# Kernel tuning notes

Measured on AMD Instinct MI355X. Metric: run time of the kernel, lower is better.

The kernel has to match this reference:

```python
import jax, jax.numpy as jnp
import numpy as np

B, N, H, E, L = 64, 100, 128, 128, 3  # batch, nodes, node_hidden, edge_hidden, gcn layers


def setup_inputs() -> dict:
    key = jax.random.key(0)
    ks = jax.random.split(key, 12)
    s = 0.05
    return dict(
        node=jax.random.normal(ks[0], (B, N, 2), jnp.float32),
        demand=jax.random.uniform(ks[1], (B, N), jnp.float32),
        dis=jax.random.uniform(ks[2], (B, N, N), jnp.float32),
        Wn0=jax.random.normal(ks[3], (3, H), jnp.float32) * s,
        bn0=jnp.zeros((H,), jnp.float32),
        Ws=jax.random.normal(ks[4], (L, H, H), jnp.float32) * s,
        Wngh=jax.random.normal(ks[5], (L, H, H), jnp.float32) * s,
        We=jax.random.normal(ks[6], (E,), jnp.float32) * s,
        be=jnp.zeros((E,), jnp.float32),
        Wih=jax.random.normal(ks[7], (2, H, 3 * H), jnp.float32) * s,
        Whh=jax.random.normal(ks[8], (2, H, 3 * H), jnp.float32) * s,
        bih=jnp.zeros((2, 3 * H), jnp.float32),
        bhh=jnp.zeros((2, 3 * H), jnp.float32),
        Wq=jax.random.normal(ks[9], (H, H), jnp.float32) * s,
        Wc=jax.random.normal(ks[10], (E, 2), jnp.float32) * s,
        bc=jnp.zeros((2,), jnp.float32),
    )


def _gru(xin, h, Wih, Whh, bih, bhh):
    gi = xin @ Wih + bih
    gh = h @ Whh + bhh
    ir, iz, inn = jnp.split(gi, 3, -1)
    hr, hz, hn = jnp.split(gh, 3, -1)
    r = jax.nn.sigmoid(ir + hr)
    z = jax.nn.sigmoid(iz + hz)
    n = jnp.tanh(inn + r * hn)
    return (1.0 - z) * n + z * h


def _decode(x, Wih, Whh, bih, bhh, Wq, sample, key):
    b, n, h = x.shape
    scale = 1.0 / np.sqrt(h).astype(np.float32)

    def step(carry, _):
        last, hid, k = carry
        emb = x[jnp.arange(b), last]                      # [b,h]
        h0 = _gru(emb, hid[0], Wih[0], Whh[0], bih[0], bhh[0])
        h1 = _gru(h0, hid[1], Wih[1], Whh[1], bih[1], bhh[1])
        logits = jnp.einsum('bh,bnh->bn', h1 @ Wq, x) * scale
        logp = jax.nn.log_softmax(logits, -1)
        k, sk = jax.random.split(k)
        if sample:
            ind = jax.random.categorical(sk, logits)
        else:
            ind = jnp.argmax(logits, -1)
        ind = ind.astype(jnp.int32)
        chosen = jnp.take_along_axis(logp, ind[:, None], 1)[:, 0]
        return (ind, jnp.stack([h0, h1]), k), (ind, chosen)

    init = (jnp.zeros((b,), jnp.int32), jnp.zeros((2, b, h), x.dtype), key)
    _, (inds, lps) = jax.lax.scan(step, init, None, length=n - 1)
    solution = jnp.concatenate([jnp.zeros((b, 1), jnp.int32), inds.T], axis=1)  # depot 0 first
    return lps.T, solution  # logprob [b,n-1], solution [b,n]


def _count_dist(sol, dis):
    bidx = jnp.arange(sol.shape[0])[:, None]
    return dis[bidx, sol[:, :-1], sol[:, 1:]].sum(axis=1, keepdims=True)  # [b,1]


def reference(node, demand, dis, Wn0, bn0, Ws, Wngh, We, be, Wih, Whh, bih, bhh, Wq, Wc, bc):
    # --- GCN encoder ---
    h = jax.nn.relu(jnp.concatenate([node, demand[..., None]], -1) @ Wn0 + bn0)  # [B,N,H]
    A = jax.nn.softmax(-dis, -1)  # distance-based soft adjacency
    for l in range(Ws.shape[0]):
        h = jax.nn.relu(h @ Ws[l] + jnp.einsum('bij,bjh->bih', A, h @ Wngh[l]))
    e = jax.nn.relu(dis[..., None] * We + be)  # [B,N,N,E]

    key = jax.random.key(42)
    k1, _ = jax.random.split(key)
    sample_logprob, sample_solution = _decode(h, Wih, Whh, bih, bhh, Wq, True, k1)
    sample_distance = _count_dist(sample_solution, dis)
    _, greedy_solution = _decode(h, Wih, Whh, bih, bhh, Wq, False, k1)
    greedy_distance = _count_dist(greedy_solution, dis)

    predict_matrix = jax.nn.softmax(e @ Wc + bc, -1)  # [B,N,N,2]

    b, n = h.shape[0], h.shape[1]
    bidx = jnp.arange(b)[:, None]
    greedy_solution_matrix = (
        jnp.zeros((b, n, n), jnp.int32)
        .at[bidx, greedy_solution[:, :-1], greedy_solution[:, 1:]]
        .set(1)
    )
    return (sample_logprob, sample_distance, greedy_distance, predict_matrix, greedy_solution_matrix)
```

## Files before the change

kernel.cpp:

```cpp
#include <hip/hip_runtime.h>
#include <math.h>

#define BB 64
#define NN 100
#define HH 128
#define T3 384

#define O0 0
#define O1 6336
#define O2 6400
#define O3 6464
#define O4 1286464

#define TINYF 1.17549435e-38f
#define SCALEF 0.08838834764831845f

__device__ __forceinline__ unsigned rotl32(unsigned x, int d) {
    return (x << d) | (x >> (32 - d));
}

__device__ __forceinline__ void tf2x32(unsigned ks0, unsigned ks1,
                                       unsigned x0, unsigned x1,
                                       unsigned& o0, unsigned& o1) {
    unsigned ks2 = ks0 ^ ks1 ^ 0x1BD11BDAu;
    x0 += ks0; x1 += ks1;
    x0 += x1; x1 = rotl32(x1, 13); x1 ^= x0;
    x0 += x1; x1 = rotl32(x1, 15); x1 ^= x0;
    x0 += x1; x1 = rotl32(x1, 26); x1 ^= x0;
    x0 += x1; x1 = rotl32(x1, 6);  x1 ^= x0;
    x0 += ks1; x1 += ks2 + 1u;
    x0 += x1; x1 = rotl32(x1, 17); x1 ^= x0;
    x0 += x1; x1 = rotl32(x1, 29); x1 ^= x0;
    x0 += x1; x1 = rotl32(x1, 16); x1 ^= x0;
    x0 += x1; x1 = rotl32(x1, 24); x1 ^= x0;
    x0 += ks2; x1 += ks0 + 2u;
    x0 += x1; x1 = rotl32(x1, 13); x1 ^= x0;
    x0 += x1; x1 = rotl32(x1, 15); x1 ^= x0;
    x0 += x1; x1 = rotl32(x1, 26); x1 ^= x0;
    x0 += x1; x1 = rotl32(x1, 6);  x1 ^= x0;
    x0 += ks0; x1 += ks1 + 3u;
    x0 += x1; x1 = rotl32(x1, 17); x1 ^= x0;
    x0 += x1; x1 = rotl32(x1, 29); x1 ^= x0;
    x0 += x1; x1 = rotl32(x1, 16); x1 ^= x0;
    x0 += x1; x1 = rotl32(x1, 24); x1 ^= x0;
    x0 += ks1; x1 += ks2 + 4u;
    x0 += x1; x1 = rotl32(x1, 13); x1 ^= x0;
    x0 += x1; x1 = rotl32(x1, 15); x1 ^= x0;
    x0 += x1; x1 = rotl32(x1, 26); x1 ^= x0;
// ... 122 lines not shown
                          const float* __restrict__ be, const float* __restrict__ Wc,
                          const float* __restrict__ bc, float* __restrict__ out3) {
    __shared__ float sWe[128], sbe[128], sc0[128], sc1[128];
    int tid = threadIdx.x;
    if (tid < 128) {
        sWe[tid] = We[tid];
        sbe[tid] = be[tid];
        sc0[tid] = Wc[tid * 2];
        sc1[tid] = Wc[tid * 2 + 1];
    }
    __syncthreads();
    float b0 = bc[0], b1 = bc[1];
    for (int pos = blockIdx.x * 256 + tid; pos < BB * NN * NN; pos += gridDim.x * 256) {
        float d = dis[pos];
        float a0 = b0, a1 = b1;
        for (int k = 0; k < 128; k++) {
            float e = fmaxf(d * sWe[k] + sbe[k], 0.0f);
            a0 += e * sc0[k];
            a1 += e * sc1[k];
        }
        float m = fmaxf(a0, a1);
        float p0 = expf(a0 - m), p1 = expf(a1 - m);
        float inv = 1.0f / (p0 + p1);
        out3[pos * 2]     = p0 * inv;
        out3[pos * 2 + 1] = p1 * inv;
    }
}

__global__ void k_zero(float* __restrict__ p, int n) {
    int i = blockIdx.x * 256 + threadIdx.x;
    if (i < n) p[i] = 0.0f;
}

__device__ __forceinline__ void matvec_tile4(const float* __restrict__ W,
                                             const float* __restrict__ hp,
                                             int nk4,
                                             float* __restrict__ pg0,
                                             float* __restrict__ pg1) {
    float a00 = 0.f, a01 = 0.f, a02 = 0.f, a03 = 0.f;
    float a10 = 0.f, a11 = 0.f, a12 = 0.f, a13 = 0.f;
#pragma unroll 4
    for (int k4 = 0; k4 < nk4; ++k4) {
        float4 hA = *(const float4*)(hp + 4 * k4);
        float4 hB = *(const float4*)(hp + 132 + 4 * k4);
        const float* Wk = W + (size_t)(4 * k4) * T3;
        float4 w0 = *(const float4*)(Wk);
        float4 w1 = *(const float4*)(Wk + T3);
        float4 w2 = *(const float4*)(Wk + 2 * T3);
        float4 w3 = *(const float4*)(Wk + 3 * T3);
        a00 += hA.x * w0.x; a01 += hA.x * w0.y; a02 += hA.x * w0.z; a03 += hA.x * w0.w;
        a10 += hB.x * w0.x; a11 += hB.x * w0.y; a12 += hB.x * w0.z; a13 += hB.x * w0.w;
        a00 += hA.y * w1.x; a01 += hA.y * w1.y; a02 += hA.y * w1.z; a03 += hA.y * w1.w;
        a10 += hB.y * w1.x; a11 += hB.y * w1.y; a12 += hB.y * w1.z; a13 += hB.y * w1.w;
        a00 += hA.z * w2.x; a01 += hA.z * w2.y; a02 += hA.z * w2.z; a03 += hA.z * w2.w;
        a10 += hB.z * w2.x; a11 += hB.z * w2.y; a12 += hB.z * w2.z; a13 += hB.z * w2.w;
        a00 += hA.w * w3.x; a01 += hA.w * w3.y; a02 += hA.w * w3.z; a03 += hA.w * w3.w;
        a10 += hB.w * w3.x; a11 += hB.w * w3.y; a12 += hB.w * w3.z; a13 += hB.w * w3.w;
    }
    float4 o;
    o.x = a00; o.y = a01; o.z = a02; o.w = a03;
    *(float4*)pg0 = o;
    o.x = a10; o.y = a11; o.z = a12; o.w = a13;
    *(float4*)pg1 = o;
}

__global__ __launch_bounds__(512, 2) void k_decode4(
    const float* __restrict__ P0,
    const float* __restrict__ Z,
    const float* __restrict__ dis,
    const float* __restrict__ Wih,
    const float* __restrict__ Whh,
    const float* __restrict__ bih,
    const float* __restrict__ bhh,
    float* __restrict__ out) {
    __shared__ float Zs[NN * 132];
    __shared__ float h0s[2 * 132], h1s[2 * 132];
    __shared__ float gi0s[2 * 384];
    __shared__ float pgA[2 * 2 * 392];
    __shared__ float pgB[2 * 2 * 392];
    __shared__ float pgC[4 * 2 * 392];
    __shared__ float sbhh0[T3], sbih1[T3], sbhh1[T3];
    __shared__ float pl[2 * 2 * 100];
    __shared__ float gum[128];
    __shared__ int s_ind2[2];

    const int tid = threadIdx.x;
    const int b = blockIdx.x;

    const float* __restrict__ Wih1 = Wih + 128 * T3;

    for (int i4 = tid; i4 < NN * 32; i4 += 512) {
        int r = i4 >> 5, c4 = (i4 & 31) * 4;
        *(float4*)&Zs[r * 132 + c4] = *(const float4*)&Z[(b * NN + r) * 128 + c4];
    }
    if (tid < T3) {
        sbhh0[tid] = bhh[tid];
        sbih1[tid] = bih[T3 + tid];
        sbhh1[tid] = bhh[T3 + tid];
    }
    if (tid < 256) {
        int m = tid >> 7, i = tid & 127;
        h0s[m * 132 + i] = 0.0f;
        h1s[m * 132 + i] = 0.0f;
    }
    if (tid == 0) { s_ind2[0] = 0; s_ind2[1] = 0; }

    unsigned kk0, kk1;
    tf2x32(0u, 42u, 0u, 0u, kk0, kk1);

    int lastm = 0;
    float dist = 0.0f;
    __syncthreads();

    for (int t = 0; t < NN - 1; t++) {
        if (tid < 384) {
            const int unit = tid / 192;
            const int r = tid - unit * 192;
            const int ks = r / 96, j4 = r - ks * 96;
            const int j0 = j4 * 4, k0 = ks * 64;
            const float* W = Whh + unit * (128 * T3) + (size_t)k0 * T3 + j0;
            const float* hp = ((unit == 0) ? h0s : h1s) + k0;
            float* pg = (unit == 0) ? pgA : pgB;
            matvec_tile4(W, hp, 16,
                         &pg[(ks * 2 + 0) * 392 + j0],
                         &pg[(ks * 2 + 1) * 392 + j0]);
        } else {
            int u = tid - 384;
            int l0 = s_ind2[0], l1 = s_ind2[1];
#pragma unroll
            for (int q = 0; q < 6; q++) {
                int f = u + 128 * q;
                int m = (f >= 384) ? 1 : 0;
                int j = f - m * 384;
                gi0s[f] = P0[(size_t)(b * NN + (m ? l1 : l0)) * T3 + j];
            }
            unsigned sk0, sk1, nk0, nk1;
            tf2x32(kk0, kk1, 0u, 1u, sk0, sk1);
            tf2x32(kk0, kk1, 0u, 0u, nk0, nk1);
            kk0 = nk0; kk1 = nk1;
            if (u < NN) gum[u] = gumbel_f(sk0, sk1, (unsigned)(b * NN + u));
        }
        __syncthreads();

        if (tid < 256) {
            int m = tid >> 7, i = tid & 127;
            float ghr = pgA[(0 * 2 + m) * 392 + i]       + pgA[(1 * 2 + m) * 392 + i]       + sbhh0[i];
            float ghz = pgA[(0 * 2 + m) * 392 + i + 128] + pgA[(1 * 2 + m) * 392 + i + 128] + sbhh0[i + 128];
            float ghn = pgA[(0 * 2 + m) * 392 + i + 256] + pgA[(1 * 2 + m) * 392 + i + 256] + sbhh0[i + 256];
            float rr = 1.0f / (1.0f + expf(-(gi0s[m * 384 + i] + ghr)));
            float zz = 1.0f / (1.0f + expf(-(gi0s[m * 384 + i + 128] + ghz)));
            float nn = tanhf(gi0s[m * 384 + i + 256] + rr * ghn);
            h0s[m * 132 + i] = (1.0f - zz) * nn + zz * h0s[m * 132 + i];
        }
        __syncthreads();

        if (tid < 384) {
            const int ks = tid / 96, j4 = tid - ks * 96;
            const int j0 = j4 * 4, k0 = ks * 32;
            const float* W = Wih1 + (size_t)k0 * T3 + j0;
            matvec_tile4(W, h0s + k0, 8,
                         &pgC[(ks * 2 + 0) * 392 + j0],
                         &pgC[(ks * 2 + 1) * 392 + j0]);
        }
        __syncthreads();

        if (tid < 256) {
            int m = tid >> 7, i = tid & 127;
            float gir = sbih1[i], giz = sbih1[i + 128], gin = sbih1[i + 256];
#pragma unroll
            for (int ks = 0; ks < 4; ks++) {
                int pb = (ks * 2 + m) * 392;
                gir += pgC[pb + i];
                giz += pgC[pb + i + 128];
                gin += pgC[pb + i + 256];
            }
            float ghr = pgB[(0 * 2 + m) * 392 + i]       + pgB[(1 * 2 + m) * 392 + i]       + sbhh1[i];
            float ghz = pgB[(0 * 2 + m) * 392 + i + 128] + pgB[(1 * 2 + m) * 392 + i + 128] + sbhh1[i + 128];
            float ghn = pgB[(0 * 2 + m) * 392 + i + 256] + pgB[(1 * 2 + m) * 392 + i + 256] + sbhh1[i + 256];
            float rr = 1.0f / (1.0f + expf(-(gir + ghr)));
            float zz = 1.0f / (1.0f + expf(-(giz + ghz)));
            float nn = tanhf(gin + rr * ghn);
            h1s[m * 132 + i] = (1.0f - zz) * nn + zz * h1s[m * 132 + i];
        }
        __syncthreads();

        if (tid < 200) {
            int ks = tid / 100, n = tid - ks * 100;
            int k0 = ks * 64;
            const float* Zp = &Zs[n * 132 + k0];
            const float* hp = &h1s[k0];
            float a0 = 0.f, a1 = 0.f;
#pragma unroll 4
            for (int q = 0; q < 16; q++) {
                float4 z4 = *(const float4*)(Zp + 4 * q);
                float4 hA = *(const float4*)(hp + 4 * q);
                float4 hB = *(const float4*)(hp + 132 + 4 * q);
                a0 += hA.x * z4.x; a0 += hA.y * z4.y; a0 += hA.z * z4.z; a0 += hA.w * z4.w;
                a1 += hB.x * z4.x; a1 += hB.y * z4.y; a1 += hB.z * z4.z; a1 += hB.w * z4.w;
            }
            pl[(0 * 2 + ks) * 100 + n] = a0;
            pl[(1 * 2 + ks) * 100 + n] = a1;
        }
        __syncthreads();

        if (tid < 128) {
            const int m = tid >> 6, lane = tid & 63;
            float v0, v1 = -__builtin_inff();
            v0 = (pl[(m * 2 + 0) * 100 + lane] + pl[(m * 2 + 1) * 100 + lane]) * SCALEF;
            if (lane + 64 < NN)
                v1 = (pl[(m * 2 + 0) * 100 + lane + 64] + pl[(m * 2 + 1) * 100 + lane + 64]) * SCALEF;
            float mx = fmaxf(v0, v1);
            for (int off = 32; off > 0; off >>= 1) mx = fmaxf(mx, __shfl_xor(mx, off));
            float e = expf(v0 - mx) + ((lane + 64 < NN) ? expf(v1 - mx) : 0.0f);
            for (int off = 32; off > 0; off >>= 1) e += __shfl_xor(e, off);
            float a0 = v0, a1 = v1;
            if (m == 0) {
                a0 += gum[lane];
                if (lane + 64 < NN) a1 += gum[lane + 64];
            }
            float bv; int bi;
            if (a1 > a0) { bv = a1; bi = lane + 64; } else { bv = a0; bi = lane; }
            for (int off = 32; off > 0; off >>= 1) {
                float ov = __shfl_xor(bv, off);
                int   oi = __shfl_xor(bi, off);
                if (ov > bv || (ov == bv && oi < bi)) { bv = ov; bi = oi; }
            }
            int ind = bi;
            float la = __shfl(v0, ind & 63);
            float lb = __shfl(v1, ind & 63);
            float lv = (ind < 64) ? la : lb;
            if (lane == 0) {
                if (m == 0) out[O0 + b * (NN - 1) + t] = lv - mx - logf(e);
                else        out[O4 + (size_t)b * NN * NN + lastm * NN + ind] = 1.0f;
                s_ind2[m] = ind;
            }
            dist += dis[b * NN * NN + lastm * NN + ind];
            lastm = ind;
        }
        __syncthreads();
    }

    if (tid == 0)  out[O1 + b] = dist;
    if (tid == 64) out[O2 + b] = dist;
}

__global__ __launch_bounds__(768) void k_decode2(
    const float* __restrict__ P0, const float* __restrict__ Z,
    const float* __restrict__ dis,
    const float* __restrict__ Wih, const float* __restrict__ Whh,
    const float* __restrict__ bih, const float* __restrict__ bhh,
    float* __restrict__ out) {
    __shared__ float Zs[NN * 129];
    __shared__ float h0s[128], h1s[128];
    __shared__ float gi0s[T3];
    __shared__ float pg0[2 * T3];
    __shared__ float gi1s[T3], gh1s[T3];
    __shared__ float sbhh0[T3], sbih1[T3], sbhh1[T3];
    __shared__ float plx[4 * NN];
    __shared__ float logits[NN];
    __shared__ float s_m, s_s;
    __shared__ int s_ind;

    const int tid = threadIdx.x;
    const int b = blockIdx.x >> 1;
    const int greedy = blockIdx.x & 1;

    const float* Whh0 = Whh;
    const float* Wih1 = Wih + 128 * T3;
    const float* Whh1 = Whh + 128 * T3;

    for (int idx = tid; idx < NN * 128; idx += 768) {
        int r = idx >> 7, c = idx & 127;
        Zs[r * 129 + c] = Z[(b * NN + r) * 128 + c];
    }
    if (tid < T3) {
        sbhh0[tid] = bhh[tid];
        sbih1[tid] = bih[T3 + tid];
        sbhh1[tid] = bhh[T3 + tid];
    }
    if (tid < 128) { h0s[tid] = 0.0f; h1s[tid] = 0.0f; }

    unsigned kk0, kk1;
    tf2x32(0u, 42u, 0u, 0u, kk0, kk1);

    int last = 0;
    float dist = 0.0f;
    __syncthreads();

    for (int t = 0; t < NN - 1; t++) {
        unsigned sk0, sk1, nk0, nk1;
        tf2x32(kk0, kk1, 0u, 1u, sk0, sk1);
        tf2x32(kk0, kk1, 0u, 0u, nk0, nk1);
        kk0 = nk0; kk1 = nk1;

        {
            const float* P0row = P0 + (size_t)(b * NN + last) * T3;
            if (tid < T3) {
                int j = tid;
                float acc = 0.0f;
                for (int k = 0; k < 64; k++) acc += h0s[k] * Whh0[k * T3 + j];
                pg0[j] = acc;
                gi0s[j] = P0row[j];
            } else {
                int j = tid - T3;
                float acc = 0.0f;
                for (int k = 64; k < 128; k++) acc += h0s[k] * Whh0[k * T3 + j];
                pg0[T3 + j] = acc;
            }
        }
        __syncthreads();
        if (tid < 128) {
            float ghr = pg0[tid] + pg0[T3 + tid] + sbhh0[tid];
            float ghz = pg0[tid + 128] + pg0[T3 + tid + 128] + sbhh0[tid + 128];
            float ghn = pg0[tid + 256] + pg0[T3 + tid + 256] + sbhh0[tid + 256];
            float r = 1.0f / (1.0f + expf(-(gi0s[tid] + ghr)));
            float z = 1.0f / (1.0f + expf(-(gi0s[tid + 128] + ghz)));
            float n = tanhf(gi0s[tid + 256] + r * ghn);
            h0s[tid] = (1.0f - z) * n + z * h0s[tid];
        }
        __syncthreads();
        if (tid < T3) {
            int j = tid;
            float acc = sbih1[j];
            for (int k = 0; k < 128; k++) acc += h0s[k] * Wih1[k * T3 + j];
            gi1s[j] = acc;
        } else {
            int j = tid - T3;
            float acc = sbhh1[j];
            for (int k = 0; k < 128; k++) acc += h1s[k] * Whh1[k * T3 + j];
            gh1s[j] = acc;
        }
        __syncthreads();
        if (tid < 128) {
            float r = 1.0f / (1.0f + expf(-(gi1s[tid] + gh1s[tid])));
            float z = 1.0f / (1.0f + expf(-(gi1s[tid + 128] + gh1s[tid + 128])));
            float n = tanhf(gi1s[tid + 256] + r * gh1s[tid + 256]);
            h1s[tid] = (1.0f - z) * n + z * h1s[tid];
        }
        __syncthreads();
        if (tid < 400) {
            int n = tid % 100, p = tid / 100;
            int k0 = p * 32;
            float acc = 0.0f;
            for (int kk = 0; kk < 32; kk++) acc += h1s[k0 + kk] * Zs[n * 129 + k0 + kk];
            plx[p * 100 + n] = acc;
        }
        __syncthreads();
        if (tid < 64) {
            float v0 = -__builtin_inff(), v1 = -__builtin_inff();
            {
                int n = tid;
                v0 = (plx[n] + plx[100 + n] + plx[200 + n] + plx[300 + n]) * SCALEF;
                logits[n] = v0;
            }
            if (tid + 64 < NN) {
                int n = tid + 64;
                v1 = (plx[n] + plx[100 + n] + plx[200 + n] + plx[300 + n]) * SCALEF;
                logits[n] = v1;
            }
            float m = fmaxf(v0, v1);
            for (int off = 32; off > 0; off >>= 1) m = fmaxf(m, __shfl_xor(m, off));
            float e = expf(v0 - m) + ((tid + 64 < NN) ? expf(v1 - m) : 0.0f);
            for (int off = 32; off > 0; off >>= 1) e += __shfl_xor(e, off);
            float a0 = v0, a1 = v1;
            if (!greedy) {
                a0 = v0 + gumbel_f(sk0, sk1, (unsigned)(b * NN + tid));
                if (tid + 64 < NN) a1 = v1 + gumbel_f(sk0, sk1, (unsigned)(b * NN + tid + 64));
            }
            float bv; int bi;
            if (a1 > a0) { bv = a1; bi = tid + 64; } else { bv = a0; bi = tid; }
            for (int off = 32; off > 0; off >>= 1) {
                float ov = __shfl_xor(bv, off);
                int   oi = __shfl_xor(bi, off);
                if (ov > bv || (ov == bv && oi < bi)) { bv = ov; bi = oi; }
            }
            if (tid == 0) { s_m = m; s_s = e; s_ind = bi; }
        }
        __syncthreads();
        int ind = s_ind;
        if (tid == 0) {
            if (!greedy) out[O0 + b * (NN - 1) + t] = logits[ind] - s_m - logf(s_s);
            dist += dis[b * NN * NN + last * NN + ind];
            if (greedy) out[O4 + b * NN * NN + last * NN + ind] = 1.0f;
        }
        last = ind;
        __syncthreads();
    }
    if (tid == 0) {
        if (!greedy) out[O1 + b] = dist;
        else         out[O2 + b] = dist;
    }
}

extern "C" void kernel_launch(void* const* d_in, const int* in_sizes, int n_in,
                              void* d_out, int out_size, void* d_ws, size_t ws_size,
                              hipStream_t stream) {
    (void)in_sizes; (void)n_in; (void)out_size;
    const float* node   = (const float*)d_in[0];
    const float* demand = (const float*)d_in[1];
    const float* dis    = (const float*)d_in[2];
    const float* Wn0    = (const float*)d_in[3];
    const float* bn0    = (const float*)d_in[4];
    const float* Ws     = (const float*)d_in[5];
    const float* Wngh   = (const float*)d_in[6];
    const float* We     = (const float*)d_in[7];
    const float* be     = (const float*)d_in[8];
    const float* Wih    = (const float*)d_in[9];
    const float* Whh    = (const float*)d_in[10];
    const float* bih    = (const float*)d_in[11];
    const float* bhh    = (const float*)d_in[12];
    const float* Wq     = (const float*)d_in[13];
    const float* Wc     = (const float*)d_in[14];
    const float* bc     = (const float*)d_in[15];
    float* out = (float*)d_out;
    float* ws  = (float*)d_ws;

    float* hA  = ws;
    float* hB  = ws + 819200;
    float* hw  = ws + 1638400;
    float* A   = ws + 2457600;
    float* P0  = ws + 2457600;
    float* WqT = ws + 4915200;
    const size_t need_bytes = (size_t)4931584 * 4;
    const bool big_ws = ws_size >= need_bytes;

    hipLaunchKernelGGL(k_embed, dim3(3200), dim3(256), 0, stream, node, demand, Wn0, bn0, hA);
    hipLaunchKernelGGL(k_adj, dim3(6400), dim3(64), 0, stream, dis, A);

    float* cur = hA;
    float* nxt = hB;
    for (int l = 0; l < 3; l++) {
        hipLaunchKernelGGL(k_hw, dim3(800), dim3(256), 0, stream, cur, Wngh + l * 16384, hw);
        hipLaunchKernelGGL(k_agg, dim3(1600), dim3(256), 0, stream, cur, Ws + l * 16384, A, hw, nxt);
        float* tswap = cur; cur = nxt; nxt = tswap;
    }

    hipLaunchKernelGGL(k_predict, dim3(2500), dim3(256), 0, stream, dis, We, be, Wc, bc, out + O3);
    hipLaunchKernelGGL(k_zero, dim3(2500), dim3(256), 0, stream, out + O4, BB * NN * NN);

    hipLaunchKernelGGL(k_transpose128, dim3(64), dim3(256), 0, stream, Wq, WqT);
    hipLaunchKernelGGL(k_hw, dim3(800), dim3(256), 0, stream, cur, WqT, hw);
    hipLaunchKernelGGL(k_mm384, dim3(800, 3), dim3(256), 0, stream, cur, Wih, bih, P0);
    if (big_ws) {
        hipLaunchKernelGGL(k_decode4, dim3(64), dim3(512), 0, stream,
                           P0, hw, dis, Wih, Whh, bih, bhh, out);
    } else {
        hipLaunchKernelGGL(k_decode2, dim3(128), dim3(768), 0, stream,
                           P0, hw, dis, Wih, Whh, bih, bhh, out);
    }
}
```

Baseline: 979.8 us.

## Keep recurrent GRU weights resident in registers across decode steps

The decode kernel now has each of 512 threads load a 16x6 slice of both Whh matrices into registers once, instead of re-reading them from global memory every step. The matvec work is repartitioned into 8 k-groups by 64 j-groups, with the partial sums reduced in shared memory. The Gumbel noise and the P0 prefetch move into other phases so all threads share the matvec work. Holding 192 floats per thread raises register pressure under launch_bounds(512,2), which risks spilling, and the larger partial-sum buffers use more shared memory.

```diff
diff --git a/kernel.cpp b/kernel.cpp
--- a/kernel.cpp
+++ b/kernel.cpp
@@ -202,39 +202,7 @@
     if (i < n) p[i] = 0.0f;
 }
 
-__device__ __forceinline__ void matvec_tile4(const float* __restrict__ W,
-                                             const float* __restrict__ hp,
-                                             int nk4,
-                                             float* __restrict__ pg0,
-                                             float* __restrict__ pg1) {
-    float a00 = 0.f, a01 = 0.f, a02 = 0.f, a03 = 0.f;
-    float a10 = 0.f, a11 = 0.f, a12 = 0.f, a13 = 0.f;
-#pragma unroll 4
-    for (int k4 = 0; k4 < nk4; ++k4) {
-        float4 hA = *(const float4*)(hp + 4 * k4);
-        float4 hB = *(const float4*)(hp + 132 + 4 * k4);
-        const float* Wk = W + (size_t)(4 * k4) * T3;
-        float4 w0 = *(const float4*)(Wk);
-        float4 w1 = *(const float4*)(Wk + T3);
-        float4 w2 = *(const float4*)(Wk + 2 * T3);
-        float4 w3 = *(const float4*)(Wk + 3 * T3);
-        a00 += hA.x * w0.x; a01 += hA.x * w0.y; a02 += hA.x * w0.z; a03 += hA.x * w0.w;
-        a10 += hB.x * w0.x; a11 += hB.x * w0.y; a12 += hB.x * w0.z; a13 += hB.x * w0.w;
-        a00 += hA.y * w1.x; a01 += hA.y * w1.y; a02 += hA.y * w1.z; a03 += hA.y * w1.w;
-        a10 += hB.y * w1.x; a11 += hB.y * w1.y; a12 += hB.y * w1.z; a13 += hB.y * w1.w;
-        a00 += hA.z * w2.x; a01 += hA.z * w2.y; a02 += hA.z * w2.z; a03 += hA.z * w2.w;
-        a10 += hB.z * w2.x; a11 += hB.z * w2.y; a12 += hB.z * w2.z; a13 += hB.z * w2.w;
-        a00 += hA.w * w3.x; a01 += hA.w * w3.y; a02 += hA.w * w3.z; a03 += hA.w * w3.w;
-        a10 += hB.w * w3.x; a11 += hB.w * w3.y; a12 += hB.w * w3.z; a13 += hB.w * w3.w;
-    }
-    float4 o;
-    o.x = a00; o.y = a01; o.z = a02; o.w = a03;
-    *(float4*)pg0 = o;
-    o.x = a10; o.y = a11; o.z = a12; o.w = a13;
-    *(float4*)pg1 = o;
-}
-
-__global__ __launch_bounds__(512, 2) void k_decode4(
+__global__ __launch_bounds__(512, 2) void k_decode5(
     const float* __restrict__ P0,
     const float* __restrict__ Z,
     const float* __restrict__ dis,
@@ -246,9 +214,8 @@
     __shared__ float Zs[NN * 132];
     __shared__ float h0s[2 * 132], h1s[2 * 132];
     __shared__ float gi0s[2 * 384];
-    __shared__ float pgA[2 * 2 * 392];
-    __shared__ float pgB[2 * 2 * 392];
-    __shared__ float pgC[4 * 2 * 392];
+    __shared__ float pgA[8 * 2 * 392];
+    __shared__ float pgB[8 * 2 * 392];
     __shared__ float sbhh0[T3], sbih1[T3], sbhh1[T3];
     __shared__ float pl[2 * 2 * 100];
     __shared__ float gum[128];
@@ -256,8 +223,27 @@
 
     const int tid = threadIdx.x;
     const int b = blockIdx.x;
+    const int kg = tid >> 6;
+    const int jg = tid & 63;
+    const int k0 = kg * 16, j0 = jg * 6;
 
     const float* __restrict__ Wih1 = Wih + 128 * T3;
+
+    float wA[16][6], wB[16][6];
+    {
+        const float* WAp = Whh + (size_t)k0 * T3 + j0;
+        const float* WBp = Whh + 128 * T3 + (size_t)k0 * T3 + j0;
+#pragma unroll
+        for (int k = 0; k < 16; k++) {
+#pragma unroll
+            for (int q = 0; q < 3; q++) {
+                float2 a = *(const float2*)(WAp + (size_t)k * T3 + 2 * q);
+                wA[k][2 * q] = a.x; wA[k][2 * q + 1] = a.y;
+                float2 c = *(const float2*)(WBp + (size_t)k * T3 + 2 * q);
+                wB[k][2 * q] = c.x; wB[k][2 * q + 1] = c.y;
+            }
+        }
+    }
 
     for (int i4 = tid; i4 < NN * 32; i4 += 512) {
         int r = i4 >> 5, c4 = (i4 & 31) * 4;
@@ -283,40 +269,84 @@
     __syncthreads();
 
     for (int t = 0; t < NN - 1; t++) {
+        unsigned sk0, sk1, nkA, nkB;
+        tf2x32(kk0, kk1, 0u, 1u, sk0, sk1);
+        tf2x32(kk0, kk1, 0u, 0u, nkA, nkB);
+        kk0 = nkA; kk1 = nkB;
+
+        float pf0 = 0.f, pf1 = 0.f;
+        int pf_m = 0, pf_j = 0;
         if (tid < 384) {
-            const int unit = tid / 192;
-            const int r = tid - unit * 192;
-            const int ks = r / 96, j4 = r - ks * 96;
-            const int j0 = j4 * 4, k0 = ks * 64;
-            const float* W = Whh + unit * (128 * T3) + (size_t)k0 * T3 + j0;
-            const float* hp = ((unit == 0) ? h0s : h1s) + k0;
-            float* pg = (unit == 0) ? pgA : pgB;
-            matvec_tile4(W, hp, 16,
-                         &pg[(ks * 2 + 0) * 392 + j0],
-                         &pg[(ks * 2 + 1) * 392 + j0]);
-        } else {
-            int u = tid - 384;
-            int l0 = s_ind2[0], l1 = s_ind2[1];
-#pragma unroll
-            for (int q = 0; q < 6; q++) {
-                int f = u + 128 * q;
-                int m = (f >= 384) ? 1 : 0;
-                int j = f - m * 384;
-                gi0s[f] = P0[(size_t)(b * NN + (m ? l1 : l0)) * T3 + j];
-            }
-            unsigned sk0, sk1, nk0, nk1;
-            tf2x32(kk0, kk1, 0u, 1u, sk0, sk1);
-            tf2x32(kk0, kk1, 0u, 0u, nk0, nk1);
-            kk0 = nk0; kk1 = nk1;
-            if (u < NN) gum[u] = gumbel_f(sk0, sk1, (unsigned)(b * NN + u));
+            pf_m = (tid >= 192);
+            pf_j = (tid - pf_m * 192) * 2;
+            float2 g2 = *(const float2*)&P0[(size_t)(b * NN + s_ind2[pf_m]) * T3 + pf_j];
+            pf0 = g2.x; pf1 = g2.y;
+        }
+
+        {
+            float acc0[6], acc1[6];
+#pragma unroll
+            for (int j = 0; j < 6; j++) { acc0[j] = 0.f; acc1[j] = 0.f; }
+#pragma unroll
+            for (int q = 0; q < 4; q++) {
+                float4 ha = *(const float4*)&h0s[k0 + 4 * q];
+                float4 hb = *(const float4*)&h0s[132 + k0 + 4 * q];
+#pragma unroll
+                for (int j = 0; j < 6; j++) {
+                    acc0[j] += wA[4 * q + 0][j] * ha.x + wA[4 * q + 1][j] * ha.y
+                             + wA[4 * q + 2][j] * ha.z + wA[4 * q + 3][j] * ha.w;
+                    acc1[j] += wA[4 * q + 0][j] * hb.x + wA[4 * q + 1][j] * hb.y
+                             + wA[4 * q + 2][j] * hb.z + wA[4 * q + 3][j] * hb.w;
+                }
+            }
+#pragma unroll
+            for (int q = 0; q < 3; q++) {
+                float2 o0; o0.x = acc0[2 * q]; o0.y = acc0[2 * q + 1];
+                *(float2*)&pgA[(kg * 2 + 0) * 392 + j0 + 2 * q] = o0;
+                float2 o1; o1.x = acc1[2 * q]; o1.y = acc1[2 * q + 1];
+                *(float2*)&pgA[(kg * 2 + 1) * 392 + j0 + 2 * q] = o1;
+            }
+        }
+        {
+            float acc0[6], acc1[6];
+#pragma unroll
+            for (int j = 0; j < 6; j++) { acc0[j] = 0.f; acc1[j] = 0.f; }
+#pragma unroll
+            for (int q = 0; q < 4; q++) {
+                float4 ha = *(const float4*)&h1s[k0 + 4 * q];
+                float4 hb = *(const float4*)&h1s[132 + k0 + 4 * q];
+#pragma unroll
+                for (int j = 0; j < 6; j++) {
+                    acc0[j] += wB[4 * q + 0][j] * ha.x + wB[4 * q + 1][j] * ha.y
+                             + wB[4 * q + 2][j] * ha.z + wB[4 * q + 3][j] * ha.w;
+                    acc1[j] += wB[4 * q + 0][j] * hb.x + wB[4 * q + 1][j] * hb.y
+                             + wB[4 * q + 2][j] * hb.z + wB[4 * q + 3][j] * hb.w;
+                }
+            }
+#pragma unroll
+            for (int q = 0; q < 3; q++) {
+                float2 o0; o0.x = acc0[2 * q]; o0.y = acc0[2 * q + 1];
+                *(float2*)&pgB[(kg * 2 + 0) * 392 + j0 + 2 * q] = o0;
+                float2 o1; o1.x = acc1[2 * q]; o1.y = acc1[2 * q + 1];
+                *(float2*)&pgB[(kg * 2 + 1) * 392 + j0 + 2 * q] = o1;
+            }
+        }
+        if (tid < 384) {
+            gi0s[pf_m * 384 + pf_j] = pf0;
+            gi0s[pf_m * 384 + pf_j + 1] = pf1;
         }
         __syncthreads();
 
         if (tid < 256) {
             int m = tid >> 7, i = tid & 127;
-            float ghr = pgA[(0 * 2 + m) * 392 + i]       + pgA[(1 * 2 + m) * 392 + i]       + sbhh0[i];
-            float ghz = pgA[(0 * 2 + m) * 392 + i + 128] + pgA[(1 * 2 + m) * 392 + i + 128] + sbhh0[i + 128];
-            float ghn = pgA[(0 * 2 + m) * 392 + i + 256] + pgA[(1 * 2 + m) * 392 + i + 256] + sbhh0[i + 256];
+            float ghr = sbhh0[i], ghz = sbhh0[i + 128], ghn = sbhh0[i + 256];
+#pragma unroll
+            for (int g = 0; g < 8; g++) {
+                int pb = (g * 2 + m) * 392;
+                ghr += pgA[pb + i];
+                ghz += pgA[pb + i + 128];
+                ghn += pgA[pb + i + 256];
+            }
             float rr = 1.0f / (1.0f + expf(-(gi0s[m * 384 + i] + ghr)));
             float zz = 1.0f / (1.0f + expf(-(gi0s[m * 384 + i + 128] + ghz)));
             float nn = tanhf(gi0s[m * 384 + i + 256] + rr * ghn);
@@ -324,29 +354,54 @@
         }
         __syncthreads();
 
-        if (tid < 384) {
-            const int ks = tid / 96, j4 = tid - ks * 96;
-            const int j0 = j4 * 4, k0 = ks * 32;
-            const float* W = Wih1 + (size_t)k0 * T3 + j0;
-            matvec_tile4(W, h0s + k0, 8,
-                         &pgC[(ks * 2 + 0) * 392 + j0],
-                         &pgC[(ks * 2 + 1) * 392 + j0]);
+        {
+            float acc0[6], acc1[6];
+#pragma unroll
+            for (int j = 0; j < 6; j++) { acc0[j] = 0.f; acc1[j] = 0.f; }
+#pragma unroll
+            for (int q = 0; q < 4; q++) {
+                float4 ha = *(const float4*)&h0s[k0 + 4 * q];
+                float4 hb = *(const float4*)&h0s[132 + k0 + 4 * q];
+#pragma unroll
+                for (int kk2 = 0; kk2 < 4; kk2++) {
+                    const float* wp = Wih1 + (size_t)(k0 + 4 * q + kk2) * T3 + j0;
+                    float2 w01 = *(const float2*)(wp);
+                    float2 w23 = *(const float2*)(wp + 2);
+                    float2 w45 = *(const float2*)(wp + 4);
+                    float hx = (kk2 == 0) ? ha.x : (kk2 == 1) ? ha.y : (kk2 == 2) ? ha.z : ha.w;
+                    float hy = (kk2 == 0) ? hb.x : (kk2 == 1) ? hb.y : (kk2 == 2) ? hb.z : hb.w;
+                    acc0[0] += w01.x * hx; acc0[1] += w01.y * hx;
+                    acc0[2] += w23.x * hx; acc0[3] += w23.y * hx;
+                    acc0[4] += w45.x * hx; acc0[5] += w45.y * hx;
+                    acc1[0] += w01.x * hy; acc1[1] += w01.y * hy;
+                    acc1[2] += w23.x * hy; acc1[3] += w23.y * hy;
+                    acc1[4] += w45.x * hy; acc1[5] += w45.y * hy;
+                }
+            }
+#pragma unroll
+            for (int q = 0; q < 3; q++) {
+                float2 o0; o0.x = acc0[2 * q]; o0.y = acc0[2 * q + 1];
+                *(float2*)&pgA[(kg * 2 + 0) * 392 + j0 + 2 * q] = o0;
+                float2 o1; o1.x = acc1[2 * q]; o1.y = acc1[2 * q + 1];
+                *(float2*)&pgA[(kg * 2 + 1) * 392 + j0 + 2 * q] = o1;
+            }
         }
         __syncthreads();
 
         if (tid < 256) {
             int m = tid >> 7, i = tid & 127;
             float gir = sbih1[i], giz = sbih1[i + 128], gin = sbih1[i + 256];
-#pragma unroll
-            for (int ks = 0; ks < 4; ks++) {
-                int pb = (ks * 2 + m) * 392;
-                gir += pgC[pb + i];
-                giz += pgC[pb + i + 128];
-                gin += pgC[pb + i + 256];
-            }
-            float ghr = pgB[(0 * 2 + m) * 392 + i]       + pgB[(1 * 2 + m) * 392 + i]       + sbhh1[i];
-            float ghz = pgB[(0 * 2 + m) * 392 + i + 128] + pgB[(1 * 2 + m) * 392 + i + 128] + sbhh1[i + 128];
-            float ghn = pgB[(0 * 2 + m) * 392 + i + 256] + pgB[(1 * 2 + m) * 392 + i + 256] + sbhh1[i + 256];
+            float ghr = sbhh1[i], ghz = sbhh1[i + 128], ghn = sbhh1[i + 256];
+#pragma unroll
+            for (int g = 0; g < 8; g++) {
+                int pa = (g * 2 + m) * 392;
+                gir += pgA[pa + i];
+                giz += pgA[pa + i + 128];
+                gin += pgA[pa + i + 256];
+                ghr += pgB[pa + i];
+                ghz += pgB[pa + i + 128];
+                ghn += pgB[pa + i + 256];
+            }
             float rr = 1.0f / (1.0f + expf(-(gir + ghr)));
             float zz = 1.0f / (1.0f + expf(-(giz + ghz)));
             float nn = tanhf(gin + rr * ghn);
@@ -356,9 +411,9 @@
 
         if (tid < 200) {
             int ks = tid / 100, n = tid - ks * 100;
-            int k0 = ks * 64;
-            const float* Zp = &Zs[n * 132 + k0];
-            const float* hp = &h1s[k0];
+            int kk0p = ks * 64;
+            const float* Zp = &Zs[n * 132 + kk0p];
+            const float* hp = &h1s[kk0p];
             float a0 = 0.f, a1 = 0.f;
 #pragma unroll 4
             for (int q = 0; q < 16; q++) {
@@ -370,6 +425,9 @@
             }
             pl[(0 * 2 + ks) * 100 + n] = a0;
             pl[(1 * 2 + ks) * 100 + n] = a1;
+        } else if (tid >= 256 && tid < 356) {
+            int u = tid - 256;
+            gum[u] = gumbel_f(sk0, sk1, (unsigned)(b * NN + u));
         }
         __syncthreads();
 
@@ -612,7 +670,7 @@
     hipLaunchKernelGGL(k_hw, dim3(800), dim3(256), 0, stream, cur, WqT, hw);
     hipLaunchKernelGGL(k_mm384, dim3(800, 3), dim3(256), 0, stream, cur, Wih, bih, P0);
     if (big_ws) {
-        hipLaunchKernelGGL(k_decode4, dim3(64), dim3(512), 0, stream,
+        hipLaunchKernelGGL(k_decode5, dim3(64), dim3(512), 0, stream,
                            P0, hw, dis, Wih, Whh, bih, bhh, out);
     } else {
         hipLaunchKernelGGL(k_decode2, dim3(128), dim3(768), 0, stream,
```

After: 1.710 ms. 1.74x slower.

## Split each batch's decode across four cooperating blocks with global flag sync

Applied to the files above, without the earlier changes.

Adds a decode kernel in which each batch element's sequential GRU decode is spread over four blocks. Each block owns a quarter of the hidden units and exchanges partial hidden states and logits through global memory, using atomic counters as inter-block barriers twice per step. Blocks are mapped to XCDs so the four partners share one. The aim is more parallelism and shorter per-step latency than one block per batch element, at the cost of spin-wait synchronisation and a deadlock risk if all 256 blocks are not co-resident.

```diff
diff --git a/kernel.cpp b/kernel.cpp
--- a/kernel.cpp
+++ b/kernel.cpp
@@ -14,6 +14,9 @@
 
 #define TINYF 1.17549435e-38f
 #define SCALEF 0.08838834764831845f
+
+#define HIDX(k) ((((k) >> 4) * 20) + ((k) & 15))
+#define HSTR 160
 
 __device__ __forceinline__ unsigned rotl32(unsigned x, int d) {
     return (x << d) | (x >> (32 - d));
@@ -202,6 +205,306 @@
     if (i < n) p[i] = 0.0f;
 }
 
+__global__ __launch_bounds__(256, 2) void k_decode7(
+    const float* __restrict__ P0,
+    const float* __restrict__ Z,
+    const float* __restrict__ dis,
+    const float* __restrict__ Wih,
+    const float* __restrict__ Whh,
+    const float* __restrict__ bih,
+    const float* __restrict__ bhh,
+    float* __restrict__ xch,
+    unsigned* __restrict__ flags,
+    float* __restrict__ out) {
+    __shared__ float ZqT[32 * 100];
+    __shared__ float h0s[2 * HSTR], h1s[2 * HSTR];
+    __shared__ float h0q[2 * 32], h1q[2 * 32];
+    __shared__ float gi0[2 * 96];
+    __shared__ float pgA[8 * 2 * 100];
+    __shared__ float pgB[8 * 2 * 100];
+    __shared__ float pgC[8 * 2 * 100];
+    __shared__ float sb_hh0[96], sb_ih1[96], sb_hh1[96];
+    __shared__ float logits[2 * 100];
+    __shared__ float gum[100];
+    __shared__ int s_ind2[2];
+
+    const int tid = threadIdx.x;
+    const int nblk = blockIdx.x;
+    const int xcd = nblk & 7, slot = nblk >> 3;
+    const int g = xcd * 8 + (slot & 7);
+    const int s = slot >> 3;
+    const int b = g;
+
+    const float* __restrict__ Whh0 = Whh;
+    const float* __restrict__ Whh1 = Whh + 128 * T3;
+    const float* __restrict__ Wih1 = Wih + 128 * T3;
+    unsigned* flag = flags + g * 32;
+
+    const int jq = tid >> 3, ks = tid & 7;
+    const int run = jq >> 3, j4 = jq & 7;
+    const int jabs = run * 128 + 32 * s + j4 * 4;
+    const int jloc = run * 32 + j4 * 4;
+    const int kb = ks * 16;
+
+    for (int i = tid; i < 3200; i += 256) {
+        int c = i / 100, n = i - c * 100;
+        ZqT[i] = Z[(b * NN + n) * 128 + 32 * s + c];
+    }
+    if (tid < 96) {
+        int r = tid >> 5, il = tid & 31;
+        int ja = r * 128 + 32 * s + il;
+        sb_hh0[tid] = bhh[ja];
+        sb_ih1[tid] = bih[T3 + ja];
+        sb_hh1[tid] = bhh[T3 + ja];
+    }
+    if (tid < 256) {
+        int m = tid >> 7, k = tid & 127;
+        h0s[m * HSTR + HIDX(k)] = 0.0f;
+        h1s[m * HSTR + HIDX(k)] = 0.0f;
+    }
+    if (tid == 0) { s_ind2[0] = 0; s_ind2[1] = 0; }
+
+    unsigned kk0 = 0, kk1 = 0;
+    tf2x32(0u, 42u, 0u, 0u, kk0, kk1);
+
+    int lastm = 0;
+    float dist = 0.0f;
+    __syncthreads();
+
+    for (int t = 0; t < NN - 1; t++) {
+        const int par = t & 1;
+        float* xg  = xch + ((size_t)(par * 64 + g)) * 1536;
+        float* xh0 = xg;
+        float* xh1 = xg + 256;
+        float* xlp = xg + 512;
+
+        if (tid < 192) {
+            float4 hA[2][4], hB[2][4];
+#pragma unroll
+            for (int m = 0; m < 2; m++)
+#pragma unroll
+                for (int q = 0; q < 4; q++) {
+                    hA[m][q] = *(const float4*)&h0s[m * HSTR + ks * 20 + 4 * q];
+                    hB[m][q] = *(const float4*)&h1s[m * HSTR + ks * 20 + 4 * q];
+                }
+            float a0[2][4], a1[2][4];
+#pragma unroll
+            for (int m = 0; m < 2; m++)
+#pragma unroll
+                for (int j = 0; j < 4; j++) { a0[m][j] = 0.f; a1[m][j] = 0.f; }
+#pragma unroll
+            for (int q = 0; q < 4; q++) {
+#pragma unroll
+                for (int kk = 0; kk < 4; kk++) {
+                    int k = kb + 4 * q + kk;
+                    float4 w0 = *(const float4*)&Whh0[(size_t)k * T3 + jabs];
+                    float4 w1 = *(const float4*)&Whh1[(size_t)k * T3 + jabs];
+                    float hA0 = (kk == 0) ? hA[0][q].x : (kk == 1) ? hA[0][q].y : (kk == 2) ? hA[0][q].z : hA[0][q].w;
+                    float hA1 = (kk == 0) ? hA[1][q].x : (kk == 1) ? hA[1][q].y : (kk == 2) ? hA[1][q].z : hA[1][q].w;
+                    float hB0 = (kk == 0) ? hB[0][q].x : (kk == 1) ? hB[0][q].y : (kk == 2) ? hB[0][q].z : hB[0][q].w;
+                    float hB1 = (kk == 0) ? hB[1][q].x : (kk == 1) ? hB[1][q].y : (kk == 2) ? hB[1][q].z : hB[1][q].w;
+                    a0[0][0] += w0.x * hA0; a0[0][1] += w0.y * hA0; a0[0][2] += w0.z * hA0; a0[0][3] += w0.w * hA0;
+                    a0[1][0] += w0.x * hA1; a0[1][1] += w0.y * hA1; a0[1][2] += w0.z * hA1; a0[1][3] += w0.w * hA1;
+                    a1[0][0] += w1.x * hB0; a1[0][1] += w1.y * hB0; a1[0][2] += w1.z * hB0; a1[0][3] += w1.w * hB0;
+                    a1[1][0] += w1.x * hB1; a1[1][1] += w1.y * hB1; a1[1][2] += w1.z * hB1; a1[1][3] += w1.w * hB1;
+                }
+            }
+#pragma unroll
+            for (int m = 0; m < 2; m++) {
+                float4 o;
+                o.x = a0[m][0]; o.y = a0[m][1]; o.z = a0[m][2]; o.w = a0[m][3];
+                *(float4*)&pgA[(ks * 2 + m) * 100 + jloc] = o;
+                o.x = a1[m][0]; o.y = a1[m][1]; o.z = a1[m][2]; o.w = a1[m][3];
+                *(float4*)&pgB[(ks * 2 + m) * 100 + jloc] = o;
+            }
+        } else {
+            int u = tid - 192;
+            unsigned sk0, sk1, nkA, nkB;
+            tf2x32(kk0, kk1, 0u, 1u, sk0, sk1);
+            tf2x32(kk0, kk1, 0u, 0u, nkA, nkB);
+            kk0 = nkA; kk1 = nkB;
+            if (u < 48) {
+                int m = u / 24, q = u - m * 24;
+                int r = q >> 3, jj4 = q & 7;
+                int ja = r * 128 + 32 * s + jj4 * 4;
+                float4 g4 = *(const float4*)&P0[(size_t)(b * NN + s_ind2[m]) * T3 + ja];
+                *(float4*)&gi0[m * 96 + r * 32 + jj4 * 4] = g4;
+            }
+            for (int u2 = u; u2 < NN; u2 += 64)
+                gum[u2] = gumbel_f(sk0, sk1, (unsigned)(b * NN + u2));
+        }
+        __syncthreads();
+
+        if (tid < 64) {
+            int m = tid >> 5, il = tid & 31;
+            int i = 32 * s + il;
+            float ghr = sb_hh0[il], ghz = sb_hh0[32 + il], ghn = sb_hh0[64 + il];
+#pragma unroll
+            for (int k8 = 0; k8 < 8; k8++) {
+                int pb = (k8 * 2 + m) * 100;
+                ghr += pgA[pb + il];
+                ghz += pgA[pb + 32 + il];
+                ghn += pgA[pb + 64 + il];
+            }
+            float rr = 1.0f / (1.0f + expf(-(gi0[m * 96 + il] + ghr)));
+            float zz = 1.0f / (1.0f + expf(-(gi0[m * 96 + 32 + il] + ghz)));
+            float nn = tanhf(gi0[m * 96 + 64 + il] + rr * ghn);
+            float hnew = (1.0f - zz) * nn + zz * h0s[m * HSTR + HIDX(i)];
+            h0q[m * 32 + il] = hnew;
+            __hip_atomic_store(&xh0[(s * 2 + m) * 32 + il], hnew,
+                               __ATOMIC_RELAXED, __HIP_MEMORY_SCOPE_AGENT);
+        }
+        __syncthreads();
+        if (tid == 0) {
+            __hip_atomic_fetch_add(flag, 1u, __ATOMIC_ACQ_REL, __HIP_MEMORY_SCOPE_AGENT);
+            unsigned tgt = 8u * t + 4u;
+            while (__hip_atomic_load(flag, __ATOMIC_ACQUIRE, __HIP_MEMORY_SCOPE_AGENT) < tgt)
+                __builtin_amdgcn_s_sleep(2);
+        }
+        __syncthreads();
+        {
+            int ss = tid >> 6, rem = tid & 63, m = rem >> 5, il = rem & 31;
+            float v = __hip_atomic_load(&xh0[(ss * 2 + m) * 32 + il],
+                                        __ATOMIC_RELAXED, __HIP_MEMORY_SCOPE_AGENT);
+            int k = ss * 32 + il;
+            h0s[m * HSTR + HIDX(k)] = v;
+        }
+        __syncthreads();
+
+        if (tid < 192) {
+            float4 hA[2][4];
+#pragma unroll
+            for (int m = 0; m < 2; m++)
+#pragma unroll
+                for (int q = 0; q < 4; q++)
+                    hA[m][q] = *(const float4*)&h0s[m * HSTR + ks * 20 + 4 * q];
+            float a0[2][4];
+#pragma unroll
+            for (int m = 0; m < 2; m++)
+#pragma unroll
+                for (int j = 0; j < 4; j++) a0[m][j] = 0.f;
+#pragma unroll
+            for (int q = 0; q < 4; q++) {
+#pragma unroll
+                for (int kk = 0; kk < 4; kk++) {
+                    int k = kb + 4 * q + kk;
+                    float4 w = *(const float4*)&Wih1[(size_t)k * T3 + jabs];
+                    float h0v = (kk == 0) ? hA[0][q].x : (kk == 1) ? hA[0][q].y : (kk == 2) ? hA[0][q].z : hA[0][q].w;
+                    float h1v = (kk == 0) ? hA[1][q].x : (kk == 1) ? hA[1][q].y : (kk == 2) ? hA[1][q].z : hA[1][q].w;
+                    a0[0][0] += w.x * h0v; a0[0][1] += w.y * h0v; a0[0][2] += w.z * h0v; a0[0][3] += w.w * h0v;
+                    a0[1][0] += w.x * h1v; a0[1][1] += w.y * h1v; a0[1][2] += w.z * h1v; a0[1][3] += w.w * h1v;
+                }
+            }
+#pragma unroll
+            for (int m = 0; m < 2; m++) {
+                float4 o;
+                o.x = a0[m][0]; o.y = a0[m][1]; o.z = a0[m][2]; o.w = a0[m][3];
+                *(float4*)&pgC[(ks * 2 + m) * 100 + jloc] = o;
+            }
+        }
+        __syncthreads();
+
+        if (tid < 64) {
+            int m = tid >> 5, il = tid & 31;
+            int i = 32 * s + il;
+            float gir = sb_ih1[il], giz = sb_ih1[32 + il], gin = sb_ih1[64 + il];
+            float ghr = sb_hh1[il], ghz = sb_hh1[32 + il], ghn = sb_hh1[64 + il];
+#pragma unroll
+            for (int k8 = 0; k8 < 8; k8++) {
+                int pb = (k8 * 2 + m) * 100;
+                gir += pgC[pb + il];
+                giz += pgC[pb + 32 + il];
+                gin += pgC[pb + 64 + il];
+                ghr += pgB[pb + il];
+                ghz += pgB[pb + 32 + il];
+                ghn += pgB[pb + 64 + il];
+            }
+            float rr = 1.0f / (1.0f + expf(-(gir + ghr)));
+            float zz = 1.0f / (1.0f + expf(-(giz + ghz)));
+            float nn = tanhf(gin + rr * ghn);
+            float hnew = (1.0f - zz) * nn + zz * h1s[m * HSTR + HIDX(i)];
+            h1q[m * 32 + il] = hnew;
+            __hip_atomic_store(&xh1[(s * 2 + m) * 32 + il], hnew,
+                               __ATOMIC_RELAXED, __HIP_MEMORY_SCOPE_AGENT);
+        }
+        __syncthreads();
+
+        if (tid < 200) {
+            int mm = tid / 100, n = tid - mm * 100;
+            float acc = 0.0f;
+#pragma unroll 8
+            for (int c = 0; c < 32; c++)
+                acc += h1q[mm * 32 + c] * ZqT[c * 100 + n];
+            __hip_atomic_store(&xlp[(s * 2 + mm) * 100 + n], acc,
+                               __ATOMIC_RELAXED, __HIP_MEMORY_SCOPE_AGENT);
+        }
+        __syncthreads();
+        if (tid == 0) {
+            __hip_atomic_fetch_add(flag, 1u, __ATOMIC_ACQ_REL, __HIP_MEMORY_SCOPE_AGENT);
+            unsigned tgt = 8u * t + 8u;
+            while (__hip_atomic_load(flag, __ATOMIC_ACQUIRE, __HIP_MEMORY_SCOPE_AGENT) < tgt)
+                __builtin_amdgcn_s_sleep(2);
+        }
+        __syncthreads();
+        {
+            int ss = tid >> 6, rem = tid & 63, m = rem >> 5, il = rem & 31;
+            float v = __hip_atomic_load(&xh1[(ss * 2 + m) * 32 + il],
+                                        __ATOMIC_RELAXED, __HIP_MEMORY_SCOPE_AGENT);
+            int k = ss * 32 + il;
+            h1s[m * HSTR + HIDX(k)] = v;
+        }
+        if (tid < 200) {
+            int mm = tid / 100, n = tid - mm * 100;
+            float sum = 0.0f;
+#pragma unroll
+            for (int ss = 0; ss < 4; ss++)
+                sum += __hip_atomic_load(&xlp[(ss * 2 + mm) * 100 + n],
+                                         __ATOMIC_RELAXED, __HIP_MEMORY_SCOPE_AGENT);
+            logits[mm * 100 + n] = sum * SCALEF;
+        }
+        __syncthreads();
+
+        if (tid < 128) {
+            const int m = tid >> 6, lane = tid & 63;
+            float v0 = logits[m * 100 + lane];
+            float v1 = (lane + 64 < NN) ? logits[m * 100 + lane + 64] : -__builtin_inff();
+            float mx = fmaxf(v0, v1);
+            for (int off = 32; off > 0; off >>= 1) mx = fmaxf(mx, __shfl_xor(mx, off));
+            float e = expf(v0 - mx) + ((lane + 64 < NN) ? expf(v1 - mx) : 0.0f);
+            for (int off = 32; off > 0; off >>= 1) e += __shfl_xor(e, off);
+            float a0 = v0, a1 = v1;
+            if (m == 0) {
+                a0 += gum[lane];
+                if (lane + 64 < NN) a1 += gum[lane + 64];
+            }
+            float bv; int bi;
+            if (a1 > a0) { bv = a1; bi = lane + 64; } else { bv = a0; bi = lane; }
+            for (int off = 32; off > 0; off >>= 1) {
+                float ov = __shfl_xor(bv, off);
+                int   oi = __shfl_xor(bi, off);
+                if (ov > bv || (ov == bv && oi < bi)) { bv = ov; bi = oi; }
+            }
+            int ind = bi;
+            float la = __shfl(v0, ind & 63);
+            float lb = __shfl(v1, ind & 63);
+            float lv = (ind < 64) ? la : lb;
+            if (lane == 0) {
+                if (s == 0) {
+                    if (m == 0) out[O0 + b * (NN - 1) + t] = lv - mx - logf(e);
+                    else        out[O4 + (size_t)b * NN * NN + lastm * NN + ind] = 1.0f;
+                }
+                s_ind2[m] = ind;
+            }
+            dist += dis[b * NN * NN + lastm * NN + ind];
+            lastm = ind;
+        }
+        __syncthreads();
+    }
+
+    if (s == 0 && tid == 0)  out[O1 + b] = dist;
+    if (s == 0 && tid == 64) out[O2 + b] = dist;
+}
+
 __device__ __forceinline__ void matvec_tile4(const float* __restrict__ W,
                                              const float* __restrict__ hp,
                                              int nk4,
@@ -235,13 +538,10 @@
 }
 
 __global__ __launch_bounds__(512, 2) void k_decode4(
-    const float* __restrict__ P0,
-    const float* __restrict__ Z,
+    const float* __restrict__ P0, const float* __restrict__ Z,
     const float* __restrict__ dis,
-    const float* __restrict__ Wih,
-    const float* __restrict__ Whh,
-    const float* __restrict__ bih,
-    const float* __restrict__ bhh,
+    const float* __restrict__ Wih, const float* __restrict__ Whh,
+    const float* __restrict__ bih, const float* __restrict__ bhh,
     float* __restrict__ out) {
     __shared__ float Zs[NN * 132];
     __shared__ float h0s[2 * 132], h1s[2 * 132];
@@ -256,7 +556,6 @@
 
     const int tid = threadIdx.x;
     const int b = blockIdx.x;
-
     const float* __restrict__ Wih1 = Wih + 128 * T3;
 
     for (int i4 = tid; i4 < NN * 32; i4 += 512) {
@@ -356,9 +655,9 @@
 
         if (tid < 200) {
             int ks = tid / 100, n = tid - ks * 100;
-            int k0 = ks * 64;
-            const float* Zp = &Zs[n * 132 + k0];
-            const float* hp = &h1s[k0];
+            int kk0p = ks * 64;
+            const float* Zp = &Zs[n * 132 + kk0p];
+            const float* hp = &h1s[kk0p];
             float a0 = 0.f, a1 = 0.f;
 #pragma unroll 4
             for (int q = 0; q < 16; q++) {
@@ -412,154 +711,6 @@
 
     if (tid == 0)  out[O1 + b] = dist;
     if (tid == 64) out[O2 + b] = dist;
-}
-
-__global__ __launch_bounds__(768) void k_decode2(
-    const float* __restrict__ P0, const float* __restrict__ Z,
-    const float* __restrict__ dis,
-    const float* __restrict__ Wih, const float* __restrict__ Whh,
-    const float* __restrict__ bih, const float* __restrict__ bhh,
-    float* __restrict__ out) {
-    __shared__ float Zs[NN * 129];
-    __shared__ float h0s[128], h1s[128];
-    __shared__ float gi0s[T3];
-    __shared__ float pg0[2 * T3];
-    __shared__ float gi1s[T3], gh1s[T3];
-    __shared__ float sbhh0[T3], sbih1[T3], sbhh1[T3];
-    __shared__ float plx[4 * NN];
-    __shared__ float logits[NN];
-    __shared__ float s_m, s_s;
-    __shared__ int s_ind;
-
-    const int tid = threadIdx.x;
-    const int b = blockIdx.x >> 1;
-    const int greedy = blockIdx.x & 1;
-
-    const float* Whh0 = Whh;
-    const float* Wih1 = Wih + 128 * T3;
-    const float* Whh1 = Whh + 128 * T3;
-
-    for (int idx = tid; idx < NN * 128; idx += 768) {
-        int r = idx >> 7, c = idx & 127;
-        Zs[r * 129 + c] = Z[(b * NN + r) * 128 + c];
-    }
-    if (tid < T3) {
-        sbhh0[tid] = bhh[tid];
-        sbih1[tid] = bih[T3 + tid];
-        sbhh1[tid] = bhh[T3 + tid];
-    }
-    if (tid < 128) { h0s[tid] = 0.0f; h1s[tid] = 0.0f; }
-
-    unsigned kk0, kk1;
-    tf2x32(0u, 42u, 0u, 0u, kk0, kk1);
-
-    int last = 0;
-    float dist = 0.0f;
-    __syncthreads();
-
-    for (int t = 0; t < NN - 1; t++) {
-        unsigned sk0, sk1, nk0, nk1;
-        tf2x32(kk0, kk1, 0u, 1u, sk0, sk1);
-        tf2x32(kk0, kk1, 0u, 0u, nk0, nk1);
-        kk0 = nk0; kk1 = nk1;
-
-        {
-            const float* P0row = P0 + (size_t)(b * NN + last) * T3;
-            if (tid < T3) {
-                int j = tid;
-                float acc = 0.0f;
-                for (int k = 0; k < 64; k++) acc += h0s[k] * Whh0[k * T3 + j];
-                pg0[j] = acc;
-                gi0s[j] = P0row[j];
-            } else {
-                int j = tid - T3;
-                float acc = 0.0f;
-                for (int k = 64; k < 128; k++) acc += h0s[k] * Whh0[k * T3 + j];
-                pg0[T3 + j] = acc;
-            }
-        }
-        __syncthreads();
-        if (tid < 128) {
-            float ghr = pg0[tid] + pg0[T3 + tid] + sbhh0[tid];
-            float ghz = pg0[tid + 128] + pg0[T3 + tid + 128] + sbhh0[tid + 128];
-            float ghn = pg0[tid + 256] + pg0[T3 + tid + 256] + sbhh0[tid + 256];
-            float r = 1.0f / (1.0f + expf(-(gi0s[tid] + ghr)));
-            float z = 1.0f / (1.0f + expf(-(gi0s[tid + 128] + ghz)));
-            float n = tanhf(gi0s[tid + 256] + r * ghn);
-            h0s[tid] = (1.0f - z) * n + z * h0s[tid];
-        }
-        __syncthreads();
-        if (tid < T3) {
-            int j = tid;
-            float acc = sbih1[j];
-            for (int k = 0; k < 128; k++) acc += h0s[k] * Wih1[k * T3 + j];
-            gi1s[j] = acc;
-        } else {
-            int j = tid - T3;
-            float acc = sbhh1[j];
-            for (int k = 0; k < 128; k++) acc += h1s[k] * Whh1[k * T3 + j];
-            gh1s[j] = acc;
-        }
-        __syncthreads();
-        if (tid < 128) {
-            float r = 1.0f / (1.0f + expf(-(gi1s[tid] + gh1s[tid])));
-            float z = 1.0f / (1.0f + expf(-(gi1s[tid + 128] + gh1s[tid + 128])));
-            float n = tanhf(gi1s[tid + 256] + r * gh1s[tid + 256]);
-            h1s[tid] = (1.0f - z) * n + z * h1s[tid];
-        }
-        __syncthreads();
-        if (tid < 400) {
-            int n = tid % 100, p = tid / 100;
-            int k0 = p * 32;
-            float acc = 0.0f;
-            for (int kk = 0; kk < 32; kk++) acc += h1s[k0 + kk] * Zs[n * 129 + k0 + kk];
-            plx[p * 100 + n] = acc;
-        }
-        __syncthreads();
-        if (tid < 64) {
-            float v0 = -__builtin_inff(), v1 = -__builtin_inff();
-            {
-                int n = tid;
-                v0 = (plx[n] + plx[100 + n] + plx[200 + n] + plx[300 + n]) * SCALEF;
-                logits[n] = v0;
-            }
-            if (tid + 64 < NN) {
-                int n = tid + 64;
-                v1 = (plx[n] + plx[100 + n] + plx[200 + n] + plx[300 + n]) * SCALEF;
-                logits[n] = v1;
-            }
-            float m = fmaxf(v0, v1);
-            for (int off = 32; off > 0; off >>= 1) m = fmaxf(m, __shfl_xor(m, off));
-            float e = expf(v0 - m) + ((tid + 64 < NN) ? expf(v1 - m) : 0.0f);
-            for (int off = 32; off > 0; off >>= 1) e += __shfl_xor(e, off);
-            float a0 = v0, a1 = v1;
-            if (!greedy) {
-                a0 = v0 + gumbel_f(sk0, sk1, (unsigned)(b * NN + tid));
-                if (tid + 64 < NN) a1 = v1 + gumbel_f(sk0, sk1, (unsigned)(b * NN + tid + 64));
-            }
-            float bv; int bi;
-            if (a1 > a0) { bv = a1; bi = tid + 64; } else { bv = a0; bi = tid; }
-            for (int off = 32; off > 0; off >>= 1) {
-                float ov = __shfl_xor(bv, off);
-                int   oi = __shfl_xor(bi, off);
-                if (ov > bv || (ov == bv && oi < bi)) { bv = ov; bi = oi; }
-            }
-            if (tid == 0) { s_m = m; s_s = e; s_ind = bi; }
-        }
-        __syncthreads();
-        int ind = s_ind;
-        if (tid == 0) {
-            if (!greedy) out[O0 + b * (NN - 1) + t] = logits[ind] - s_m - logf(s_s);
-            dist += dis[b * NN * NN + last * NN + ind];
-            if (greedy) out[O4 + b * NN * NN + last * NN + ind] = 1.0f;
-        }
-        last = ind;
-        __syncthreads();
-    }
-    if (tid == 0) {
-        if (!greedy) out[O1 + b] = dist;
-        else         out[O2 + b] = dist;
-    }
 }
 
 extern "C" void kernel_launch(void* const* d_in, const int* in_sizes, int n_in,
@@ -585,14 +736,16 @@
     float* out = (float*)d_out;
     float* ws  = (float*)d_ws;
 
-    float* hA  = ws;
-    float* hB  = ws + 819200;
-    float* hw  = ws + 1638400;
-    float* A   = ws + 2457600;
-    float* P0  = ws + 2457600;
-    float* WqT = ws + 4915200;
-    const size_t need_bytes = (size_t)4931584 * 4;
-    const bool big_ws = ws_size >= need_bytes;
+    float* hA   = ws;
+    float* hB   = ws + 819200;
+    float* hw   = ws + 1638400;
+    float* A    = ws + 2457600;
+    float* P0   = ws + 2457600;
+    float* WqT  = ws + 4915200;
+    float* xch  = ws + 4931584;
+    float* flagsF = ws + 5128192;
+    const size_t need7 = (size_t)5130240 * 4;
+    const size_t need4 = (size_t)4931584 * 4;
 
     hipLaunchKernelGGL(k_embed, dim3(3200), dim3(256), 0, stream, node, demand, Wn0, bn0, hA);
     hipLaunchKernelGGL(k_adj, dim3(6400), dim3(64), 0, stream, dis, A);
@@ -611,11 +764,15 @@
     hipLaunchKernelGGL(k_transpose128, dim3(64), dim3(256), 0, stream, Wq, WqT);
     hipLaunchKernelGGL(k_hw, dim3(800), dim3(256), 0, stream, cur, WqT, hw);
     hipLaunchKernelGGL(k_mm384, dim3(800, 3), dim3(256), 0, stream, cur, Wih, bih, P0);
-    if (big_ws) {
+
+    if (ws_size >= need7) {
+        hipLaunchKernelGGL(k_zero, dim3(8), dim3(256), 0, stream, flagsF, 2048);
+        hipLaunchKernelGGL(k_decode7, dim3(256), dim3(256), 0, stream,
+                           P0, hw, dis, Wih, Whh, bih, bhh,
+                           xch, (unsigned*)flagsF, out);
+    } else {
+        (void)need4;
         hipLaunchKernelGGL(k_decode4, dim3(64), dim3(512), 0, stream,
                            P0, hw, dis, Wih, Whh, bih, bhh, out);
-    } else {
-        hipLaunchKernelGGL(k_decode2, dim3(128), dim3(768), 0, stream,
-                           P0, hw, dis, Wih, Whh, bih, bhh, out);
-    }
-}
+    }
+}
```

New measurement: 2.071 ms. +111.4%, slower.
